# Performance work log

Measured on AMD Instinct MI355X. Metric: run time of the kernel, lower is better.

The kernel has to match this reference:

```python
import jax, jax.numpy as jnp
import numpy as np

T, B, S = 32, 64, 128
V, WV, ENC, DEC, ATT = 50000, 512, 512, 512, 512
LAYERS, POOL = 2, 2
IN0 = WV + ENC  # input_feed concat


def _gru_cell(x, h, W_ih, b_ih, W_hh, b_hh):
    gi = x @ W_ih.T + b_ih
    gh = h @ W_hh.T + b_hh
    i_r, i_z, i_n = jnp.split(gi, 3, axis=-1)
    h_r, h_z, h_n = jnp.split(gh, 3, axis=-1)
    r = jax.nn.sigmoid(i_r + h_r)
    z = jax.nn.sigmoid(i_z + h_z)
    n = jnp.tanh(i_n + r * h_n)
    return (1.0 - z) * n + z * h


def setup_inputs() -> dict:
    key = jax.random.key(0)
    ks = iter(jax.random.split(key, 32))
    d = {}
    d['input'] = jax.random.randint(next(ks), (T, B), 0, V)
    d['hidden'] = jax.random.normal(next(ks), (LAYERS, B, DEC), jnp.float32)
    d['context'] = jax.random.normal(next(ks), (S, B, ENC), jnp.float32)
    d['src_pad_mask'] = jnp.zeros((B, S), jnp.float32)
    d['init_att'] = jax.random.normal(next(ks), (B, ENC), jnp.float32)
    sc = 0.05
    d['emb_W'] = jax.random.normal(next(ks), (V, WV), jnp.float32) * sc
    # stacked GRU params (layer0 input IN0, layer1 input DEC)
    d['W_ih0'] = jax.random.normal(next(ks), (3 * DEC, IN0), jnp.float32) * sc
    d['b_ih0'] = jnp.zeros((3 * DEC,), jnp.float32)
    d['W_hh0'] = jax.random.normal(next(ks), (3 * DEC, DEC), jnp.float32) * sc
    d['b_hh0'] = jnp.zeros((3 * DEC,), jnp.float32)
    d['W_ih1'] = jax.random.normal(next(ks), (3 * DEC, DEC), jnp.float32) * sc
    d['b_ih1'] = jnp.zeros((3 * DEC,), jnp.float32)
    d['W_hh1'] = jax.random.normal(next(ks), (3 * DEC, DEC), jnp.float32) * sc
    d['b_hh1'] = jnp.zeros((3 * DEC,), jnp.float32)
    # concat attention
    d['W_pre'] = jax.random.normal(next(ks), (ATT, ENC), jnp.float32) * sc
    d['b_pre'] = jnp.zeros((ATT,), jnp.float32)
    d['W_q'] = jax.random.normal(next(ks), (ATT, DEC), jnp.float32) * sc
    d['w_v'] = jax.random.normal(next(ks), (ATT,), jnp.float32) * sc
    # copy switch
    d['W_copy'] = jax.random.normal(next(ks), (1, ENC + DEC), jnp.float32) * sc
    d['b_copy'] = jnp.zeros((1,), jnp.float32)
    # readout
    d['W_read'] = jax.random.normal(next(ks), (DEC, WV + DEC + ENC), jnp.float32) * sc
    d['b_read'] = jnp.zeros((DEC,), jnp.float32)
    return d


def reference(input, hidden, context, src_pad_mask, init_att, emb_W,
              W_ih0, b_ih0, W_hh0, b_hh0, W_ih1, b_ih1, W_hh1, b_hh1,
              W_pre, b_pre, W_q, w_v, W_copy, b_copy, W_read, b_read):
    emb = emb_W[input]                     # [T,B,WV]
    ctx_bse = jnp.transpose(context, (1, 0, 2))  # [B,S,ENC]
    precompute = jnp.einsum('bse,ae->bsa', ctx_bse, W_pre) + b_pre  # [B,S,ATT]
    neg_inf = jnp.finfo(jnp.float32).min

    def step(carry, emb_t):
        h, cur_ctx = carry
        x = jnp.concatenate([emb_t, cur_ctx], axis=1)  # input_feed
        h0 = _gru_cell(x, h[0], W_ih0, b_ih0, W_hh0, b_hh0)
        out = _gru_cell(h0, h[1], W_ih1, b_ih1, W_hh1, b_hh1)
        h_new = jnp.stack([h0, out])
        # concat attention
        q = out @ W_q.T                                  # [B,ATT]
        energy = jnp.tanh(precompute + q[:, None, :]) @ w_v  # [B,S]
        energy = jnp.where(src_pad_mask > 0.5, neg_inf, energy)
        attn = jax.nn.softmax(energy, axis=-1)
        new_ctx = jnp.einsum('bs,bse->be', attn, ctx_bse)
        copy_prob = jax.nn.sigmoid(
            jnp.concatenate([out, new_ctx], axis=1) @ W_copy.T + b_copy)  # [B,1]
        readout = jnp.concatenate([emb_t, out, new_ctx], axis=1) @ W_read.T + b_read
        maxout = jnp.max(readout.reshape(B, DEC // POOL, POOL), axis=-1)  # [B,DEC/POOL]
        return (h_new, new_ctx), (maxout, attn, copy_prob)

    (hidden_f, cur_ctx_f), (g_outputs, c_outputs, copy_gates) = jax.lax.scan(
        step, (hidden, init_att), emb)
    attn_last = c_outputs[-1]
    return g_outputs, c_outputs, copy_gates, hidden_f, attn_last, cur_ctx_f
```

## Files before the change

### kernel.cpp

```cpp
#include <hip/hip_runtime.h>


typedef unsigned short u16;
typedef unsigned long long u64;
using bf16x8 = __attribute__((ext_vector_type(8))) short;
using f32x4  = __attribute__((ext_vector_type(4))) float;

#define OFF_EGI    0
#define OFF_EREAD  3145728
#define OFF_CNT    6291456
#define CNT_BYTES  101376

#define UB_PREB    8388608
#define UB_WIH0C   18087936
#define UB_WHH0    18874368
#define UB_WHH1    19660800
#define UB_WIH1    20447232
#define UB_WRO     21233664
#define UB_WRC     21495808
#define UB_CTXT    21757952
#define UB_WQ      26050560
#define ROT_H0B    26312704
#define ROT_H1B    27394048
#define ROT_CTXB   28475392

#define PH_A   0
#define PH_B   1
#define PH_CT  2

#define OO_G    0
#define OO_C    524288
#define OO_CP   786432
#define OO_HID  788480
#define OO_AL   854016
#define OO_CTXF 862208

__device__ __forceinline__ float sigm(float x) {
    return 1.0f / (1.0f + __expf(-x));
}
__device__ __forceinline__ float tanh_(float x) {
    x = fmaxf(x, -15.f);
    float e = __expf(-2.0f * x);
    return (1.0f - e) / (1.0f + e);
}
__device__ __forceinline__ u16 f2b(float x) {
    unsigned u = __float_as_uint(x);
    return (u16)((u + 0x7FFFu + ((u >> 16) & 1u)) >> 16);
}
__device__ __forceinline__ float b2f(unsigned u) {
    return __uint_as_float(u << 16);
}
__device__ __forceinline__ float bfe(bf16x8 v, int k) {
    return b2f((unsigned)(unsigned short)v[k]);
}

__device__ __forceinline__ void sta8(void* p, u64 v) {
    __hip_atomic_store((u64*)p, v, __ATOMIC_RELAXED, __HIP_MEMORY_SCOPE_AGENT);
}
__device__ __forceinline__ void sta4(void* p, unsigned v) {
    __hip_atomic_store((unsigned*)p, v, __ATOMIC_RELAXED, __HIP_MEMORY_SCOPE_AGENT);
}

__device__ __forceinline__ unsigned* cptr(float* wsf, int t, int ph, int g) {
    return (unsigned*)(wsf + OFF_CNT) + ((((t * 3) + ph) * 8 + g) << 5);
}
__device__ __forceinline__ void bar_wait1(unsigned* c, unsigned tgt) {
    if (threadIdx.x == 0) {
        while (__hip_atomic_load(c, __ATOMIC_RELAXED, __HIP_MEMORY_SCOPE_AGENT) < tgt)
            __builtin_amdgcn_s_sleep(1);
    }
    __syncthreads();
}
__device__ __forceinline__ void bar_wait8(unsigned* base, unsigned tgt) {
    if (threadIdx.x < 8) {
        unsigned* c = base + (threadIdx.x << 5);
        while (__hip_atomic_load(c, __ATOMIC_RELAXED, __HIP_MEMORY_SCOPE_AGENT) < tgt)
            __builtin_amdgcn_s_sleep(1);
    }
    __syncthreads();
}
__device__ __forceinline__ void bar_arrive(unsigned* c) {
    asm volatile("s_waitcnt vmcnt(0)" ::: "memory");
    __syncthreads();
    if (threadIdx.x == 0)
        __hip_atomic_fetch_add(c, 1u, __ATOMIC_RELAXED, __HIP_MEMORY_SCOPE_AGENT);
}

__device__ __forceinline__ void gemm64(
    const float* __restrict__ xrow, const float* __restrict__ wrow,
    int kt0, int nkt, float* lds_x, float* lds_w,
    float* __restrict__ outp, int JW, int orow0, int j0,
    const float* __restrict__ addp, int addmode, int addJW,
    u16* __restrict__ obf)
{
    const int tid = threadIdx.x;
    const int tb4 = tid >> 4, tj4 = tid & 15;
    float acc[4][4];
#pragma unroll
    for (int a = 0; a < 4; ++a)
#pragma unroll
        for (int b = 0; b < 4; ++b) acc[a][b] = 0.f;

    for (int kt = kt0; kt < kt0 + nkt; ++kt) {
        const int kb = kt << 6;
        __syncthreads();
        {
            const int rl = tid >> 2;
#pragma unroll
            for (int i = 0; i < 4; ++i) {
                const int kk = ((tid & 3) << 4) + (i << 2);
                float4 xv = *(const float4*)(xrow + kb + kk);
                float4 wv = *(const float4*)(wrow + kb + kk);
                lds_x[(kk + 0) * 64 + rl] = xv.x;
                lds_x[(kk + 1) * 64 + rl] = xv.y;
                lds_x[(kk + 2) * 64 + rl] = xv.z;
                lds_x[(kk + 3) * 64 + rl] = xv.w;
                lds_w[(kk + 0) * 64 + rl] = wv.x;
                lds_w[(kk + 1) * 64 + rl] = wv.y;
                lds_w[(kk + 2) * 64 + rl] = wv.z;
                lds_w[(kk + 3) * 64 + rl] = wv.w;
            }
        }
        __syncthreads();
#pragma unroll 4
        for (int kk = 0; kk < 64; ++kk) {
            float4 xv = *(const float4*)(lds_x + kk * 64 + tb4 * 4);
            float4 wv = *(const float4*)(lds_w + kk * 64 + tj4 * 4);
            acc[0][0] += xv.x * wv.x; acc[0][1] += xv.x * wv.y;
            acc[0][2] += xv.x * wv.z; acc[0][3] += xv.x * wv.w;
            acc[1][0] += xv.y * wv.x; acc[1][1] += xv.y * wv.y;
            acc[1][2] += xv.y * wv.z; acc[1][3] += xv.y * wv.w;
            acc[2][0] += xv.z * wv.x; acc[2][1] += xv.z * wv.y;
            acc[2][2] += xv.z * wv.z; acc[2][3] += xv.z * wv.w;
            acc[3][0] += xv.w * wv.x; acc[3][1] += xv.w * wv.y;
            acc[3][2] += xv.w * wv.z; acc[3][3] += xv.w * wv.w;
        }
    }
#pragma unroll
    for (int ib = 0; ib < 4; ++ib) {
        const int row = tb4 * 4 + ib;
        const int jc = j0 + tj4 * 4;
        float4 r;
        r.x = acc[ib][0]; r.y = acc[ib][1]; r.z = acc[ib][2]; r.w = acc[ib][3];
        if (addmode == 1) {
            float4 bv = *(const float4*)(addp + jc);
            r.x += bv.x; r.y += bv.y; r.z += bv.z; r.w += bv.w;
        } else if (addmode == 2) {
            float4 bv = *(const float4*)(addp + (size_t)(orow0 + row) * addJW + jc);
            r.x += bv.x; r.y += bv.y; r.z += bv.z; r.w += bv.w;
        }
        if (obf) {
            u64 pv = (u64)f2b(r.x) | ((u64)f2b(r.y) << 16)
                   | ((u64)f2b(r.z) << 32) | ((u64)f2b(r.w) << 48);
            *(u64*)(obf + (size_t)(orow0 + row) * 512 + jc) = pv;
        } else {
            *(float4*)(outp + (size_t)(orow0 + row) * JW + jc) = r;
        }
    }
}

__device__ __forceinline__ void stage_plain(const u16* __restrict__ Xg, u16* sX) {
    const int tid = threadIdx.x;
#pragma unroll
    for (int p = 0; p < 16; ++p) {
        const int chunk = p * 256 + tid;
        const int row = chunk >> 6, cb16 = chunk & 63;
        const int src = row * 1024 + cb16 * 16;
        const int dst = src ^ ((row & 7) << 4);
        *(float4*)((char*)sX + dst) = *(const float4*)((const char*)Xg + src);
    }
}

__device__ __forceinline__ void mfma_tile(const u16* sX, const u16* __restrict__ Wg,
                                          f32x4 acc[4]) {
    const int tid = threadIdx.x;
    const int w = tid >> 6, l15 = tid & 15, lhi = (tid & 63) >> 4;
    const int arow = w * 16 + l15;
    const char* aptr = (const char*)sX;
    const int abase = arow * 1024 + lhi * 16;
    const int aswz = (arow & 7) << 4;
#pragma unroll 4
    for (int ks = 0; ks < 16; ++ks) {
        bf16x8 a = *(const bf16x8*)(aptr + ((abase + ks * 64) ^ aswz));
        const u16* wp = Wg + l15 * 512 + ks * 32 + lhi * 8;
        acc[0] = __builtin_amdgcn_mfma_f32_16x16x32_bf16(a, *(const bf16x8*)(wp), acc[0], 0, 0, 0);
        acc[1] = __builtin_amdgcn_mfma_f32_16x16x32_bf16(a, *(const bf16x8*)(wp + 16*512), acc[1], 0, 0, 0);
        acc[2] = __builtin_amdgcn_mfma_f32_16x16x32_bf16(a, *(const bf16x8*)(wp + 32*512), acc[2], 0, 0, 0);
        acc[3] = __builtin_amdgcn_mfma_f32_16x16x32_bf16(a, *(const bf16x8*)(wp + 48*512), acc[3], 0, 0, 0);
    }
}

__device__ __forceinline__ void mfma_tile3(const u16* sX,
        const u16* __restrict__ W0, const u16* __restrict__ W1,
        const u16* __restrict__ W2, f32x4 a0[4], f32x4 a1[4], f32x4 a2[4]) {
    const int tid = threadIdx.x;
    const int w = tid >> 6, l15 = tid & 15, lhi = (tid & 63) >> 4;
    const int arow = w * 16 + l15;
    const char* aptr = (const char*)sX;
    const int abase = arow * 1024 + lhi * 16;
    const int aswz = (arow & 7) << 4;
#pragma unroll 2
    for (int ks = 0; ks < 16; ++ks) {
        bf16x8 a = *(const bf16x8*)(aptr + ((abase + ks * 64) ^ aswz));
        const int wo = l15 * 512 + ks * 32 + lhi * 8;
        const u16 *p0 = W0 + wo, *p1 = W1 + wo, *p2 = W2 + wo;
        bf16x8 b00 = *(const bf16x8*)(p0),         b01 = *(const bf16x8*)(p0 + 8192);
        bf16x8 b02 = *(const bf16x8*)(p0 + 16384), b03 = *(const bf16x8*)(p0 + 24576);
        bf16x8 b10 = *(const bf16x8*)(p1),         b11 = *(const bf16x8*)(p1 + 8192);
        bf16x8 b12 = *(const bf16x8*)(p1 + 16384), b13 = *(const bf16x8*)(p1 + 24576);
        bf16x8 b20 = *(const bf16x8*)(p2),         b21 = *(const bf16x8*)(p2 + 8192);
        bf16x8 b22 = *(const bf16x8*)(p2 + 16384), b23 = *(const bf16x8*)(p2 + 24576);
        a0[0] = __builtin_amdgcn_mfma_f32_16x16x32_bf16(a, b00, a0[0], 0, 0, 0);
        a0[1] = __builtin_amdgcn_mfma_f32_16x16x32_bf16(a, b01, a0[1], 0, 0, 0);
        a0[2] = __builtin_amdgcn_mfma_f32_16x16x32_bf16(a, b02, a0[2], 0, 0, 0);
        a0[3] = __builtin_amdgcn_mfma_f32_16x16x32_bf16(a, b03, a0[3], 0, 0, 0);
        a1[0] = __builtin_amdgcn_mfma_f32_16x16x32_bf16(a, b10, a1[0], 0, 0, 0);
        a1[1] = __builtin_amdgcn_mfma_f32_16x16x32_bf16(a, b11, a1[1], 0, 0, 0);
        a1[2] = __builtin_amdgcn_mfma_f32_16x16x32_bf16(a, b12, a1[2], 0, 0, 0);
        a1[3] = __builtin_amdgcn_mfma_f32_16x16x32_bf16(a, b13, a1[3], 0, 0, 0);
        a2[0] = __builtin_amdgcn_mfma_f32_16x16x32_bf16(a, b20, a2[0], 0, 0, 0);
        a2[1] = __builtin_amdgcn_mfma_f32_16x16x32_bf16(a, b21, a2[1], 0, 0, 0);
        a2[2] = __builtin_amdgcn_mfma_f32_16x16x32_bf16(a, b22, a2[2], 0, 0, 0);
        a2[3] = __builtin_amdgcn_mfma_f32_16x16x32_bf16(a, b23, a2[3], 0, 0, 0);
    }
}
__device__ __forceinline__ void zero4(f32x4 a[4]) {
    f32x4 z = {0.f, 0.f, 0.f, 0.f};
    a[0] = z; a[1] = z; a[2] = z; a[3] = z;
}

__global__ __launch_bounds__(256)
void k_upfront(const int* __restrict__ inp, const float* __restrict__ hid,
               const float* __restrict__ ctxin, const float* __restrict__ init_att,
               const float* __restrict__ embW,
               const float* __restrict__ W_ih0, const float* __restrict__ b_ih0,
               const float* __restrict__ W_hh0, const float* __restrict__ W_hh1,
               const float* __restrict__ W_ih1, const float* __restrict__ W_q,
               const float* __restrict__ W_read, const float* __restrict__ b_read,
               const float* __restrict__ W_pre, const float* __restrict__ b_pre,
               float* __restrict__ wsf)
{
    __shared__ float lds_x[4096], lds_w[4096];
    u16* wsu = (u16*)wsf;
    const int jid = blockIdx.x, tid = threadIdx.x, rl = tid >> 2;
    if (jid < 768) {
        const int mt = jid / 24, jt = jid % 24, j0 = jt << 6;
        const int idx = inp[mt * 64 + rl];
        gemm64(embW + (size_t)idx * 512, W_ih0 + (size_t)(j0 + rl) * 1024,
               0, 8, lds_x, lds_w, wsf + OFF_EGI, 1536, mt << 6, j0, b_ih0, 1, 0, nullptr);
    } else if (jid < 1024) {
        const int r = jid - 768, mt = r >> 3, jt = r & 7, j0 = jt << 6;
        const int idx = inp[mt * 64 + rl];
        gemm64(embW + (size_t)idx * 512, W_read + (size_t)(j0 + rl) * 1536,
               0, 8, lds_x, lds_w, wsf + OFF_EREAD, 512, mt << 6, j0, b_read, 1, 0, nullptr);
    } else if (jid < 2048) {
        const int r = jid - 1024, mt = r >> 3, jt = r & 7, j0 = jt << 6;
        const int m = (mt << 6) + rl, b = m >> 7, s = m & 127;
        gemm64(ctxin + (size_t)((s << 6) + b) * 512, W_pre + (size_t)(j0 + rl) * 512,
               0, 8, lds_x, lds_w, nullptr, 512, mt << 6, j0, b_pre, 1, 0,
               wsu + UB_PREB);
    } else if (jid < 2272) {
        const int w = jid - 2048;
        if (w < 48) {
            for (int i = 0; i < 64; ++i) {
                int e = w * 16384 + i * 256 + tid;
                int j = e >> 9, k = e & 511;
                wsu[UB_WIH0C + e] = f2b(W_ih0[(size_t)j * 1024 + 512 + k]);
            }
        } else if (w < 96) {
            for (int i = 0; i < 64; ++i) {
                int e = (w - 48) * 16384 + i * 256 + tid;
                wsu[UB_WHH0 + e] = f2b(W_hh0[e]);
            }
        } else if (w < 144) {
            for (int i = 0; i < 64; ++i) {
                int e = (w - 96) * 16384 + i * 256 + tid;
                wsu[UB_WHH1 + e] = f2b(W_hh1[e]);
            }
        } else if (w < 192) {
            for (int i = 0; i < 64; ++i) {
                int e = (w - 144) * 16384 + i * 256 + tid;
                wsu[UB_WIH1 + e] = f2b(W_ih1[e]);
            }
        } else if (w < 208) {
            for (int i = 0; i < 64; ++i) {
                int e = (w - 192) * 16384 + i * 256 + tid;
                int j = e >> 9, k = e & 511;
                wsu[UB_WRO + e] = f2b(W_read[(size_t)j * 1536 + 512 + k]);
            }
        } else {
            for (int i = 0; i < 64; ++i) {
                int e = (w - 208) * 16384 + i * 256 + tid;
                int j = e >> 9, k = e & 511;
                wsu[UB_WRC + e] = f2b(W_read[(size_t)j * 1536 + 1024 + k]);
            }
        }
    } else if (jid < 2528) {
        const int w2 = jid - 2272;
        for (int rr = 0; rr < 32; ++rr) {
            const int r = w2 * 32 + rr;
            const int b = r >> 7, s = r & 127;
            const float* src = ctxin + ((size_t)s * 64 + b) * 512;
#pragma unroll
            for (int h = 0; h < 2; ++h) {
                int e = h * 256 + tid;
                wsu[UB_CTXT + (size_t)r * 512 + e] = f2b(src[e]);
            }
        }
    } else if (jid < 2544) {
        const int w3 = jid - 2528;
        for (int i = 0; i < 64; ++i) {
            int e = w3 * 16384 + i * 256 + tid;
            wsu[UB_WQ + e] = f2b(W_q[e]);
        }
    } else {
        const int job = jid - 2544;
        const float* src = job == 0 ? hid : (job == 1 ? hid + 32768 : init_att);
        u16* dst = wsu + (size_t)(job == 0 ? ROT_H0B : (job == 1 ? ROT_H1B : ROT_CTXB))
                 + (size_t)32 * 32768;
        for (int i = 0; i < 128; ++i) {
            int e = i * 256 + tid;
            dst[e] = f2b(src[e]);
        }
    }
}

__global__ __launch_bounds__(256, 1)
void k_loop(const float* __restrict__ b_hh0, const float* __restrict__ b_ih1,
            const float* __restrict__ b_hh1, const float* __restrict__ hid,
            const float* __restrict__ maskp, const float* __restrict__ w_v,
            const float* __restrict__ W_copy, const float* __restrict__ b_copy,
            float* __restrict__ wsf, float* __restrict__ dout)
{
    __shared__ u16 sX[32768];
    u16* wsu = (u16*)wsf;
    const int blk = blockIdx.x, tid = threadIdx.x;
    const int w = tid >> 6, l15 = tid & 15, lhi = (tid & 63) >> 4;

    if (blk < 8) {
        const int j = blk;
        float hp[4][4];
#pragma unroll
        for (int cb = 0; cb < 4; ++cb)
#pragma unroll
            for (int r = 0; r < 4; ++r)
                hp[cb][r] = hid[(w * 16 + lhi * 4 + r) * 512 + j * 64 + cb * 16 + l15];

        for (int t = 0; t < 32; ++t) {
            const size_t slot = t, slotp = (t == 0) ? 32 : (size_t)(t - 1);
            float eg0[4][4], eg1[4][4], eg2[4][4];
            {
                const float* EG = wsf + OFF_EGI + (size_t)t * 98304;
#pragma unroll
                for (int cb = 0; cb < 4; ++cb) {
                    const int gc = j * 64 + cb * 16 + l15;
#pragma unroll
                    for (int r = 0; r < 4; ++r) {
                        const float* eg = EG + (size_t)(w * 16 + lhi * 4 + r) * 1536;
                        eg0[cb][r] = eg[gc];
                        eg1[cb][r] = eg[512 + gc];
                        eg2[cb][r] = eg[1024 + gc];
                    }
                }
            }
            f32x4 aR[4], aZ[4], aIN[4], aHN[4];
            zero4(aR); zero4(aZ); zero4(aIN); zero4(aHN);
            if (t > 0) bar_wait1(cptr(wsf, t - 1, PH_A, 0), 8);
            stage_plain(wsu + ROT_H0B + slotp * 32768, sX);
            __syncthreads();
            mfma_tile3(sX, wsu + UB_WHH0 + (size_t)(j * 64) * 512,
                           wsu + UB_WHH0 + (size_t)(512 + j * 64) * 512,
                           wsu + UB_WHH0 + (size_t)(1024 + j * 64) * 512, aR, aZ, aHN);
            __syncthreads();
            if (t > 0) bar_wait8(cptr(wsf, t - 1, PH_CT, 0), 8);
            stage_plain(wsu + ROT_CTXB + slotp * 32768, sX);
            __syncthreads();
            mfma_tile3(sX, wsu + UB_WIH0C + (size_t)(j * 64) * 512,
                           wsu + UB_WIH0C + (size_t)(512 + j * 64) * 512,
                           wsu + UB_WIH0C + (size_t)(1024 + j * 64) * 512, aR, aZ, aIN);
            __syncthreads();
            u16* tile = sX;
#pragma unroll
            for (int cb = 0; cb < 4; ++cb) {
                const int lc = cb * 16 + l15, gc = j * 64 + lc;
                const float brr = b_hh0[gc], bzz = b_hh0[512 + gc], bnn = b_hh0[1024 + gc];
#pragma unroll
                for (int r = 0; r < 4; ++r) {
                    const int row = w * 16 + lhi * 4 + r;
                    float rr = sigm(aR[cb][r] + eg0[cb][r] + brr);
                    float zz = sigm(aZ[cb][r] + eg1[cb][r] + bzz);
                    float nn = tanh_(aIN[cb][r] + eg2[cb][r] + rr * (aHN[cb][r] + bnn));
                    float v = (1.f - zz) * nn + zz * hp[cb][r];
                    hp[cb][r] = v;
                    tile[row * 64 + lc] = f2b(v);
                    if (t == 31) dout[OO_HID + row * 512 + gc] = v;
                }
            }
            __syncthreads();
            {
                u16* dst = wsu + ROT_H0B + slot * 32768 + j * 64;
#pragma unroll
                for (int i = 0; i < 4; ++i) {
                    int e = i * 256 + tid, row = e >> 4, c = e & 15;
                    sta8(dst + (size_t)row * 512 + c * 4, *(const u64*)(tile + row * 64 + c * 4));
                }
            }
            bar_arrive(cptr(wsf, t, PH_A, 0));
        }
    } else if (blk < 16) {
        const int j = blk - 8;
        float hp[4][4];
#pragma unroll
        for (int cb = 0; cb < 4; ++cb)
#pragma unroll
            for (int r = 0; r < 4; ++r)
                hp[cb][r] = hid[32768 + (w * 16 + lhi * 4 + r) * 512 + j * 64 + cb * 16 + l15];

        for (int t = 0; t < 32; ++t) {
            const size_t slot = t, slotp = (t == 0) ? 32 : (size_t)(t - 1);
            f32x4 aR[4], aZ[4], aIN[4], aHN[4];
            zero4(aR); zero4(aZ); zero4(aIN); zero4(aHN);
            if (t > 0) bar_wait1(cptr(wsf, t - 1, PH_B, 0), 8);
            stage_plain(wsu + ROT_H1B + slotp * 32768, sX);
            __syncthreads();
            mfma_tile3(sX, wsu + UB_WHH1 + (size_t)(j * 64) * 512,
                           wsu + UB_WHH1 + (size_t)(512 + j * 64) * 512,
                           wsu + UB_WHH1 + (size_t)(1024 + j * 64) * 512, aR, aZ, aHN);
            __syncthreads();
            bar_wait1(cptr(wsf, t, PH_A, 0), 8);
            stage_plain(wsu + ROT_H0B + slot * 32768, sX);
            __syncthreads();
            mfma_tile3(sX, wsu + UB_WIH1 + (size_t)(j * 64) * 512,
                           wsu + UB_WIH1 + (size_t)(512 + j * 64) * 512,
                           wsu + UB_WIH1 + (size_t)(1024 + j * 64) * 512, aR, aZ, aIN);
            __syncthreads();
            u16* tile = sX;
#pragma unroll
            for (int cb = 0; cb < 4; ++cb) {
                const int lc = cb * 16 + l15, gc = j * 64 + lc;
                const float bir = b_ih1[gc] + b_hh1[gc];
                const float biz = b_ih1[512 + gc] + b_hh1[512 + gc];
                const float bin_ = b_ih1[1024 + gc];
                const float bhn = b_hh1[1024 + gc];
#pragma unroll
                for (int r = 0; r < 4; ++r) {
                    const int row = w * 16 + lhi * 4 + r;
                    float rr = sigm(aR[cb][r] + bir);
                    float zz = sigm(aZ[cb][r] + biz);
                    float nn = tanh_(aIN[cb][r] + bin_ + rr * (aHN[cb][r] + bhn));
                    float v = (1.f - zz) * nn + zz * hp[cb][r];
                    hp[cb][r] = v;
                    tile[row * 64 + lc] = f2b(v);
                    if (t == 31) dout[OO_HID + 32768 + row * 512 + gc] = v;
                }
            }
            __syncthreads();
            {
                u16* dst = wsu + ROT_H1B + slot * 32768 + j * 64;
#pragma unroll
                for (int i = 0; i < 4; ++i) {
                    int e = i * 256 + tid, row = e >> 4, c = e & 15;
                    sta8(dst + (size_t)row * 512 + c * 4, *(const u64*)(tile + row * 64 + c * 4));
                }
            }
            bar_arrive(cptr(wsf, t, PH_B, 0));
        }
    } else if (blk < 80) {
        const int b = blk - 16;
        float* sf = (float*)sX;
        float* s_out  = sf;
        float* s_q    = sf + 512;
        float* s_e    = sf + 1024;
        float* s_at   = sf + 1152;
        float* s_ctx  = sf + 1280;
        float* s_red  = sf + 1792;
        float* s_part = sf + 2048;
        float* s_ctxp = sf + 2304;
        float* s_wv   = sf + 4352;
        float* s_msk  = sf + 4864;
        float* s_wcp  = sf + 4992;

        for (int i = tid; i < 512; i += 256) s_wv[i] = w_v[i];
        for (int i = tid; i < 1024; i += 256) s_wcp[i] = W_copy[i];
        if (tid < 128) s_msk[tid] = (maskp[b * 128 + tid] > 0.5f) ? -3.0e38f : 0.0f;
        __syncthreads();

        for (int t = 0; t < 32; ++t) {
            const size_t slot = t;
            bar_wait1(cptr(wsf, t, PH_B, 0), 8);
            {
                const u16* ob = wsu + ROT_H1B + slot * 32768 + b * 512;
                const int c0 = tid * 2;
                unsigned pv = *(const unsigned*)(ob + c0);
                s_out[c0] = b2f(pv & 0xffffu);
                s_out[c0 + 1] = b2f(pv >> 16);
            }
            __syncthreads();
            {
                const u16* wq0 = wsu + UB_WQ + (size_t)tid * 512;
                const u16* wq1 = wq0 + (size_t)256 * 512;
                float q0 = 0.f, q1 = 0.f;
#pragma unroll 8
                for (int i = 0; i < 64; ++i) {
                    bf16x8 w0 = *(const bf16x8*)(wq0 + i * 8);
                    bf16x8 w1 = *(const bf16x8*)(wq1 + i * 8);
#pragma unroll
                    for (int k2 = 0; k2 < 8; ++k2) {
                        float ov = s_out[i * 8 + k2];
                        q0 += ov * bfe(w0, k2);
                        q1 += ov * bfe(w1, k2);
                    }
                }
                s_q[tid] = q0; s_q[tid + 256] = q1;
            }
            __syncthreads();
            {
                const int s = tid >> 1, sh = tid & 1;
                const u16* prep = wsu + UB_PREB + (((size_t)b * 128 + s) << 9) + (sh << 8);
                float part = 0.f;
#pragma unroll 4
                for (int i = 0; i < 32; ++i) {
                    bf16x8 v = *(const bf16x8*)(prep + i * 8);
#pragma unroll
                    for (int k2 = 0; k2 < 8; ++k2) {
                        const int a = (sh << 8) + i * 8 + k2;
                        part += tanh_(bfe(v, k2) + s_q[a]) * s_wv[a];
                    }
                }
                s_part[tid] = part;
            }
            __syncthreads();
            if (tid < 128) s_e[tid] = s_part[tid * 2] + s_part[tid * 2 + 1] + s_msk[tid];
            __syncthreads();
            if (tid < 64) {
                float e0 = s_e[tid], e1 = s_e[tid + 64];
                float mx = fmaxf(e0, e1);
#pragma unroll
                for (int d2 = 1; d2 < 64; d2 <<= 1) mx = fmaxf(mx, __shfl_xor(mx, d2, 64));
                float x0 = __expf(e0 - mx), x1 = __expf(e1 - mx);
                float sm = x0 + x1;
#pragma unroll
                for (int d2 = 1; d2 < 64; d2 <<= 1) sm += __shfl_xor(sm, d2, 64);
                float inv = 1.f / sm;
                x0 *= inv; x1 *= inv;
                s_at[tid] = x0; s_at[tid + 64] = x1;
                float* co = dout + OO_C + ((size_t)t * 64 + b) * 128;
                co[tid] = x0; co[tid + 64] = x1;
                if (t == 31) {
                    dout[OO_AL + b * 128 + tid] = x0;
                    dout[OO_AL + b * 128 + tid + 64] = x1;
                }
            }
            __syncthreads();
            {
                const u16* ct = wsu + UB_CTXT + (size_t)b * 65536;
                const int ln = tid & 63;
                float ac[8] = {0.f,0.f,0.f,0.f,0.f,0.f,0.f,0.f};
#pragma unroll 4
                for (int si = 0; si < 32; ++si) {
                    const int s2 = w * 32 + si;
                    const float at = s_at[s2];
                    bf16x8 v = *(const bf16x8*)(ct + (size_t)s2 * 512 + ln * 8);
#pragma unroll
                    for (int k2 = 0; k2 < 8; ++k2) ac[k2] = fmaf(at, bfe(v, k2), ac[k2]);
                }
#pragma unroll
                for (int k2 = 0; k2 < 8; ++k2) s_ctxp[w * 512 + ln * 8 + k2] = ac[k2];
            }
            __syncthreads();
            {
                const int e0 = tid * 2;
                float c0 = s_ctxp[e0] + s_ctxp[512 + e0] + s_ctxp[1024 + e0] + s_ctxp[1536 + e0];
                float c1 = s_ctxp[e0 + 1] + s_ctxp[512 + e0 + 1] + s_ctxp[1024 + e0 + 1] + s_ctxp[1536 + e0 + 1];
                s_ctx[e0] = c0; s_ctx[e0 + 1] = c1;
                sta4(wsu + ROT_CTXB + slot * 32768 + b * 512 + e0,
                     (unsigned)f2b(c0) | ((unsigned)f2b(c1) << 16));
                if (t == 31) {
                    dout[OO_CTXF + b * 512 + e0] = c0;
                    dout[OO_CTXF + b * 512 + e0 + 1] = c1;
                }
            }
            bar_arrive(cptr(wsf, t, PH_CT, b >> 3));
            {
                const int i2 = tid * 2;
                float part = s_out[i2] * s_wcp[i2] + s_ctx[i2] * s_wcp[512 + i2]
                           + s_out[i2 + 1] * s_wcp[i2 + 1] + s_ctx[i2 + 1] * s_wcp[512 + i2 + 1];
                s_red[tid] = part;
                __syncthreads();
                for (int d2 = 128; d2 > 0; d2 >>= 1) {
                    if (tid < d2) s_red[tid] += s_red[tid + d2];
                    __syncthreads();
                }
                if (tid == 0)
                    dout[OO_CP + t * 64 + b] = sigm(s_red[0] + b_copy[0]);
            }
        }
    } else {
        const int j = blk - 80;
        for (int tp = 0; tp < 32; ++tp) {
            bar_wait1(cptr(wsf, tp, PH_B, 0), 8);
            stage_plain(wsu + ROT_H1B + (size_t)tp * 32768, sX);
            __syncthreads();
            f32x4 acc[4];
            zero4(acc);
            mfma_tile(sX, wsu + UB_WRO + (size_t)(j * 64) * 512, acc);
            bar_wait8(cptr(wsf, tp, PH_CT, 0), 8);
            __syncthreads();
            stage_plain(wsu + ROT_CTXB + (size_t)tp * 32768, sX);
            __syncthreads();
            mfma_tile(sX, wsu + UB_WRC + (size_t)(j * 64) * 512, acc);
            __syncthreads();
            float* ft = (float*)sX;
            const float* ER = wsf + OFF_EREAD + (size_t)tp * 32768;
#pragma unroll
            for (int cb = 0; cb < 4; ++cb) {
                const int lc = cb * 16 + l15;
#pragma unroll
                for (int r = 0; r < 4; ++r) {
                    const int row = w * 16 + lhi * 4 + r;
                    ft[row * 64 + lc] = acc[cb][r] + ER[(size_t)row * 512 + j * 64 + lc];
                }
            }
            __syncthreads();
#pragma unroll
            for (int i = 0; i < 8; ++i) {
                int e = i * 256 + tid, row = e >> 5, c2 = e & 31;
                dout[OO_G + (size_t)tp * 16384 + row * 256 + j * 32 + c2] =
                    fmaxf(ft[row * 64 + 2 * c2], ft[row * 64 + 2 * c2 + 1]);
            }
        }
    }
}

extern "C" void kernel_launch(void* const* d_in, const int* in_sizes, int n_in,
                              void* d_out, int out_size, void* d_ws, size_t ws_size,
                              hipStream_t stream) {
    const int*   inp      = (const int*)d_in[0];
    const float* hid      = (const float*)d_in[1];
    const float* ctxin    = (const float*)d_in[2];
    const float* maskp    = (const float*)d_in[3];
    const float* init_att = (const float*)d_in[4];
    const float* embW     = (const float*)d_in[5];
    const float* W_ih0    = (const float*)d_in[6];
    const float* b_ih0    = (const float*)d_in[7];
    const float* W_hh0    = (const float*)d_in[8];
    const float* b_hh0    = (const float*)d_in[9];
    const float* W_ih1    = (const float*)d_in[10];
    const float* b_ih1    = (const float*)d_in[11];
    const float* W_hh1    = (const float*)d_in[12];
    const float* b_hh1    = (const float*)d_in[13];
    const float* W_pre    = (const float*)d_in[14];
    const float* b_pre    = (const float*)d_in[15];
    const float* W_q      = (const float*)d_in[16];
    const float* w_v      = (const float*)d_in[17];
    const float* W_copy   = (const float*)d_in[18];
    const float* b_copy   = (const float*)d_in[19];
    const float* W_read   = (const float*)d_in[20];
    const float* b_read   = (const float*)d_in[21];
    float* dout = (float*)d_out;
    float* wsf  = (float*)d_ws;

    hipMemsetAsync((char*)d_ws + (size_t)OFF_CNT * 4, 0, CNT_BYTES, stream);

    k_upfront<<<dim3(2547), dim3(256), 0, stream>>>(
        inp, hid, ctxin, init_att, embW, W_ih0, b_ih0, W_hh0, W_hh1, W_ih1, W_q,
        W_read, b_read, W_pre, b_pre, wsf);

    k_loop<<<dim3(88), dim3(256), 0, stream>>>(
        b_hh0, b_ih1, b_hh1, hid, maskp, w_v, W_copy, b_copy, wsf, dout);
}
```

Measured before the change: 3.100 ms.

## Split attention context into separate blocks, keep precompute and context in registers

Moves the per-batch context-vector weighted sum and copy-gate computation out of the attention blocks into 64 new dedicated blocks, synchronised through a new per-batch attention-ready counter phase and an attention buffer in workspace. The attention blocks now keep their slice of the precomputed attention projection in registers, and the context blocks keep their context slice in registers, removing repeated global reads every step. W_q is stored transposed so each thread reads coalesced pairs per input element. This adds more blocks and an extra global handoff plus barrier per step, and large register arrays risk spills.

Result: slower. 4.026 ms (+29.9%).

```diff
diff --git a/kernel.cpp b/kernel.cpp
--- a/kernel.cpp
+++ b/kernel.cpp
@@ -9,7 +9,8 @@
 #define OFF_EGI    0
 #define OFF_EREAD  3145728
 #define OFF_CNT    6291456
-#define CNT_BYTES  101376
+#define CNT_BYTES  1081344
+#define OFF_ATTN   6561792
 
 #define UB_PREB    8388608
 #define UB_WIH0C   18087936
@@ -26,7 +27,8 @@
 
 #define PH_A   0
 #define PH_B   1
-#define PH_CT  2
+#define PH_AT  2
+#define PH_CT  3
 
 #define OO_G    0
 #define OO_C    524288
@@ -62,7 +64,7 @@
 }
 
 __device__ __forceinline__ unsigned* cptr(float* wsf, int t, int ph, int g) {
-    return (unsigned*)(wsf + OFF_CNT) + ((((t * 3) + ph) * 8 + g) << 5);
+    return (unsigned*)(wsf + OFF_CNT) + ((((t * 4) + ph) * 64 + g) << 5);
 }
 __device__ __forceinline__ void bar_wait1(unsigned* c, unsigned tgt) {
     if (threadIdx.x == 0) {
@@ -311,7 +313,8 @@
         const int w3 = jid - 2528;
         for (int i = 0; i < 64; ++i) {
             int e = w3 * 16384 + i * 256 + tid;
-            wsu[UB_WQ + e] = f2b(W_q[e]);
+            int k = e >> 9, rem = e & 511, a2 = rem >> 1, hi = rem & 1;
+            wsu[UB_WQ + e] = f2b(W_q[(size_t)(a2 + hi * 256) * 512 + k]);
         }
     } else {
         const int job = jid - 2544;
@@ -472,24 +475,25 @@
         float* s_q    = sf + 512;
         float* s_e    = sf + 1024;
         float* s_at   = sf + 1152;
-        float* s_ctx  = sf + 1280;
-        float* s_red  = sf + 1792;
-        float* s_part = sf + 2048;
-        float* s_ctxp = sf + 2304;
-        float* s_wv   = sf + 4352;
-        float* s_msk  = sf + 4864;
-        float* s_wcp  = sf + 4992;
+        float* s_part = sf + 1280;
+        float* s_wv   = sf + 1536;
+        float* s_msk  = sf + 2048;
 
         for (int i = tid; i < 512; i += 256) s_wv[i] = w_v[i];
-        for (int i = tid; i < 1024; i += 256) s_wcp[i] = W_copy[i];
         if (tid < 128) s_msk[tid] = (maskp[b * 128 + tid] > 0.5f) ? -3.0e38f : 0.0f;
+        const int sh = tid & 1;
+        bf16x8 pr[32];
+        {
+            const u16* prep = wsu + UB_PREB + (((size_t)b * 128 + (tid >> 1)) << 9) + (sh << 8);
+#pragma unroll
+            for (int i = 0; i < 32; ++i) pr[i] = *(const bf16x8*)(prep + i * 8);
+        }
         __syncthreads();
 
         for (int t = 0; t < 32; ++t) {
-            const size_t slot = t;
             bar_wait1(cptr(wsf, t, PH_B, 0), 8);
             {
-                const u16* ob = wsu + ROT_H1B + slot * 32768 + b * 512;
+                const u16* ob = wsu + ROT_H1B + (size_t)t * 32768 + b * 512;
                 const int c0 = tid * 2;
                 unsigned pv = *(const unsigned*)(ob + c0);
                 s_out[c0] = b2f(pv & 0xffffu);
@@ -497,30 +501,23 @@
             }
             __syncthreads();
             {
-                const u16* wq0 = wsu + UB_WQ + (size_t)tid * 512;
-                const u16* wq1 = wq0 + (size_t)256 * 512;
+                const u16* wq = wsu + UB_WQ + 2 * tid;
                 float q0 = 0.f, q1 = 0.f;
 #pragma unroll 8
-                for (int i = 0; i < 64; ++i) {
-                    bf16x8 w0 = *(const bf16x8*)(wq0 + i * 8);
-                    bf16x8 w1 = *(const bf16x8*)(wq1 + i * 8);
-#pragma unroll
-                    for (int k2 = 0; k2 < 8; ++k2) {
-                        float ov = s_out[i * 8 + k2];
-                        q0 += ov * bfe(w0, k2);
-                        q1 += ov * bfe(w1, k2);
-                    }
+                for (int k = 0; k < 512; ++k) {
+                    unsigned pv = *(const unsigned*)(wq + (size_t)k * 512);
+                    float ov = s_out[k];
+                    q0 = fmaf(ov, b2f(pv & 0xffffu), q0);
+                    q1 = fmaf(ov, b2f(pv >> 16), q1);
                 }
                 s_q[tid] = q0; s_q[tid + 256] = q1;
             }
             __syncthreads();
             {
-                const int s = tid >> 1, sh = tid & 1;
-                const u16* prep = wsu + UB_PREB + (((size_t)b * 128 + s) << 9) + (sh << 8);
                 float part = 0.f;
-#pragma unroll 4
+#pragma unroll
                 for (int i = 0; i < 32; ++i) {
-                    bf16x8 v = *(const bf16x8*)(prep + i * 8);
+                    bf16x8 v = pr[i];
 #pragma unroll
                     for (int k2 = 0; k2 < 8; ++k2) {
                         const int a = (sh << 8) + i * 8 + k2;
@@ -552,32 +549,57 @@
                 }
             }
             __syncthreads();
-            {
-                const u16* ct = wsu + UB_CTXT + (size_t)b * 65536;
-                const int ln = tid & 63;
-                float ac[8] = {0.f,0.f,0.f,0.f,0.f,0.f,0.f,0.f};
-#pragma unroll 4
-                for (int si = 0; si < 32; ++si) {
-                    const int s2 = w * 32 + si;
-                    const float at = s_at[s2];
-                    bf16x8 v = *(const bf16x8*)(ct + (size_t)s2 * 512 + ln * 8);
-#pragma unroll
-                    for (int k2 = 0; k2 < 8; ++k2) ac[k2] = fmaf(at, bfe(v, k2), ac[k2]);
-                }
-#pragma unroll
-                for (int k2 = 0; k2 < 8; ++k2) s_ctxp[w * 512 + ln * 8 + k2] = ac[k2];
-            }
-            __syncthreads();
-            {
+            if (tid < 128)
+                sta4((unsigned*)(wsf + OFF_ATTN + (size_t)t * 8192 + b * 128 + tid),
+                     __float_as_uint(s_at[tid]));
+            bar_arrive(cptr(wsf, t, PH_AT, b));
+        }
+    } else if (blk < 144) {
+        const int b = blk - 80;
+        float* sf = (float*)sX;
+        float* s_out = sf;
+        float* s_at  = sf + 512;
+        float* s_ctx = sf + 640;
+        float* s_red = sf + 1152;
+        float* s_wcp = sf + 1408;
+
+        for (int i = tid; i < 1024; i += 256) s_wcp[i] = W_copy[i];
+        unsigned cr[128];
+        {
+            const u16* ct = wsu + UB_CTXT + (size_t)b * 65536 + tid * 2;
+#pragma unroll
+            for (int s = 0; s < 128; ++s) cr[s] = *(const unsigned*)(ct + (size_t)s * 512);
+        }
+        __syncthreads();
+
+        for (int t = 0; t < 32; ++t) {
+            bar_wait1(cptr(wsf, t, PH_B, 0), 8);
+            {
+                const u16* ob = wsu + ROT_H1B + (size_t)t * 32768 + b * 512;
+                const int c0 = tid * 2;
+                unsigned pv = *(const unsigned*)(ob + c0);
+                s_out[c0] = b2f(pv & 0xffffu);
+                s_out[c0 + 1] = b2f(pv >> 16);
+            }
+            bar_wait1(cptr(wsf, t, PH_AT, b), 1);
+            if (tid < 128) s_at[tid] = wsf[OFF_ATTN + (size_t)t * 8192 + b * 128 + tid];
+            __syncthreads();
+            {
+                float a0 = 0.f, a1 = 0.f;
+#pragma unroll
+                for (int s = 0; s < 128; ++s) {
+                    float at = s_at[s];
+                    unsigned pv = cr[s];
+                    a0 = fmaf(at, b2f(pv & 0xffffu), a0);
+                    a1 = fmaf(at, b2f(pv >> 16), a1);
+                }
                 const int e0 = tid * 2;
-                float c0 = s_ctxp[e0] + s_ctxp[512 + e0] + s_ctxp[1024 + e0] + s_ctxp[1536 + e0];
-                float c1 = s_ctxp[e0 + 1] + s_ctxp[512 + e0 + 1] + s_ctxp[1024 + e0 + 1] + s_ctxp[1536 + e0 + 1];
-                s_ctx[e0] = c0; s_ctx[e0 + 1] = c1;
-                sta4(wsu + ROT_CTXB + slot * 32768 + b * 512 + e0,
-                     (unsigned)f2b(c0) | ((unsigned)f2b(c1) << 16));
+                s_ctx[e0] = a0; s_ctx[e0 + 1] = a1;
+                sta4(wsu + ROT_CTXB + (size_t)t * 32768 + b * 512 + e0,
+                     (unsigned)f2b(a0) | ((unsigned)f2b(a1) << 16));
                 if (t == 31) {
-                    dout[OO_CTXF + b * 512 + e0] = c0;
-                    dout[OO_CTXF + b * 512 + e0 + 1] = c1;
+                    dout[OO_CTXF + b * 512 + e0] = a0;
+                    dout[OO_CTXF + b * 512 + e0 + 1] = a1;
                 }
             }
             bar_arrive(cptr(wsf, t, PH_CT, b >> 3));
@@ -596,7 +618,7 @@
             }
         }
     } else {
-        const int j = blk - 80;
+        const int j = blk - 144;
         for (int tp = 0; tp < 32; ++tp) {
             bar_wait1(cptr(wsf, tp, PH_B, 0), 8);
             stage_plain(wsu + ROT_H1B + (size_t)tp * 32768, sX);
@@ -666,6 +688,6 @@
         inp, hid, ctxin, init_att, embW, W_ih0, b_ih0, W_hh0, W_hh1, W_ih1, W_q,
         W_read, b_read, W_pre, b_pre, wsf);
 
-    k_loop<<<dim3(88), dim3(256), 0, stream>>>(
+    k_loop<<<dim3(152), dim3(256), 0, stream>>>(
         b_hh0, b_ih1, b_hh1, hid, maskp, w_v, W_copy, b_copy, wsf, dout);
 }
```
